# Performance work log

Measured on AMD Instinct MI355X. Metric: run time of the kernel, lower is better.

Reference implementation:

```python
import jax, jax.numpy as jnp
import numpy as np

ITER_ROUTING = 3
EPS = 1e-9


def squash(s):
    # s: [C, H]; standard capsule squash along last dim
    norm_sq = jnp.sum(s * s, axis=-1, keepdims=True)
    return s * (norm_sq / (1.0 + norm_sq)) / jnp.sqrt(norm_sq + EPS)


def setup_inputs() -> dict:
    key = jax.random.key(0)
    k1, k2 = jax.random.split(key)
    C, K, H = 512, 64, 1024
    encoder_output = jax.random.normal(k1, (C, K, H), dtype=jnp.float32)
    # nn.Linear(H, H, bias=False) weight, scaled like kaiming-uniform-ish init
    W = jax.random.normal(k2, (H, H), dtype=jnp.float32) * (1.0 / np.sqrt(H))
    return {"encoder_output": encoder_output, "W": W}


def reference(encoder_output, W):
    C, K, H = encoder_output.shape
    # Linear projection (loop-invariant: l_1 is fixed, so hoist out of routing loop)
    # torch Linear computes x @ W.T
    hat = jnp.einsum('ckh,oh->cko', encoder_output, W)  # [C, K, H]
    b = jnp.zeros((C, K), dtype=encoder_output.dtype)
    c = None
    for _ in range(ITER_ROUTING):
        d = jax.nn.softmax(b, axis=-1)                  # [C, K]
        c_hat = jnp.einsum('ckh,ck->ch', hat, d)        # [C, H] weighted sum
        c = squash(c_hat)                               # [C, H]
        b = b + jnp.einsum('ckh,ch->ck', hat, c)        # agreement update
    return c
```

## Files before the change

### kernel.cpp

```cpp
#include <hip/hip_runtime.h>
#include <hip/hip_bf16.h>
#include <cstdint>


#define C_DIM 512
#define KCAPS 64
#define H_DIM 1024
#define M_DIM (C_DIM * KCAPS)

typedef _Float16 h8 __attribute__((ext_vector_type(8)));
typedef _Float16 h4 __attribute__((ext_vector_type(4)));
typedef float f4 __attribute__((ext_vector_type(4)));

__global__ void cvt_f32_f16(const float* __restrict__ in, _Float16* __restrict__ out, int n4) {
    int i = blockIdx.x * blockDim.x + threadIdx.x;
    int stride = gridDim.x * blockDim.x;
    for (; i < n4; i += stride) {
        float4 v = ((const float4*)in)[i];
        h4 o;
        o[0] = (_Float16)v.x; o[1] = (_Float16)v.y;
        o[2] = (_Float16)v.z; o[3] = (_Float16)v.w;
        ((h4*)out)[i] = o;
    }
}

__device__ __forceinline__ void gload16(const _Float16* g, _Float16* l) {
    __builtin_amdgcn_global_load_lds(
        (const __attribute__((address_space(1))) void*)g,
        (__attribute__((address_space(3))) void*)l, 16, 0, 0);
}

__global__ __launch_bounds__(256) void gemm_f16_bt(const _Float16* __restrict__ A,
                                                   const _Float16* __restrict__ B,
                                                   _Float16* __restrict__ Cmat) {
    __shared__ _Float16 As[128 * 64] __attribute__((aligned(16)));
    __shared__ _Float16 Bs[128 * 64] __attribute__((aligned(16)));
    const int tid  = threadIdx.x;
    const int lane = tid & 63;
    const int wid  = tid >> 6;
    const int bid  = blockIdx.x;
    const int swz  = (bid & 7) * 256 + (bid >> 3);
    const int tm   = swz >> 3;
    const int tn   = swz & 7;
    const int wr   = wid >> 1, wc = wid & 1;

    f4 acc[4][4] = {};

    const int r8 = lane >> 3;
    const int c8 = (lane & 7) * 8;

    const _Float16* Abase = A + (size_t)(tm * 128) * H_DIM;
    const _Float16* Bbase = B + (size_t)(tn * 128) * H_DIM;

    for (int kt = 0; kt < H_DIM; kt += 64) {
        #pragma unroll
        for (int i = 0; i < 4; ++i) {
            const int chunk = wid * 4 + i;
            const int row   = chunk * 8 + r8;
            gload16(Abase + (size_t)row * H_DIM + kt + c8, &As[chunk * 512]);
            gload16(Bbase + (size_t)row * H_DIM + kt + c8, &Bs[chunk * 512]);
        }
        __syncthreads();

        #pragma unroll
        for (int kk = 0; kk < 64; kk += 32) {
            h8 af[4], bf[4];
            const int kidx = kk + ((lane >> 4) << 3);
            #pragma unroll
            for (int m = 0; m < 4; ++m)
                af[m] = *(const h8*)&As[(wr * 64 + m * 16 + (lane & 15)) * 64 + kidx];
            #pragma unroll
            for (int n = 0; n < 4; ++n)
                bf[n] = *(const h8*)&Bs[(wc * 64 + n * 16 + (lane & 15)) * 64 + kidx];
            #pragma unroll
            for (int m = 0; m < 4; ++m)
                #pragma unroll
                for (int n = 0; n < 4; ++n)
                    acc[m][n] = __builtin_amdgcn_mfma_f32_16x16x32_f16(af[m], bf[n], acc[m][n], 0, 0, 0);
        }
        __syncthreads();
    }

    const int crow0 = tm * 128 + wr * 64;
    const int ccol0 = tn * 128 + wc * 64;
    #pragma unroll
    for (int m = 0; m < 4; ++m) {
        #pragma unroll
        for (int n = 0; n < 4; ++n) {
            const int col = ccol0 + n * 16 + (lane & 15);
            #pragma unroll
            for (int q = 0; q < 4; ++q) {
                const int row = crow0 + m * 16 + (lane >> 4) * 4 + q;
                Cmat[(size_t)row * H_DIM + col] = (_Float16)acc[m][n][q];
            }
        }
    }
}

__device__ __forceinline__ float2 upk(unsigned int u) {
    unsigned short ul = (unsigned short)(u & 0xffffu);
    unsigned short uh = (unsigned short)(u >> 16);
    _Float16 lo, hi;
    __builtin_memcpy(&lo, &ul, 2);
    __builtin_memcpy(&hi, &uh, 2);
    return make_float2((float)lo, (float)hi);
}

__global__ __launch_bounds__(512) void routing2(const _Float16* __restrict__ hat,
                                                float* __restrict__ out) {
    __shared__ _Float16 hat_s[KCAPS * H_DIM] __attribute__((aligned(16)));
    __shared__ float b_lds[KCAPS];
    __shared__ float d_lds[KCAPS];
    __shared__ float c_lds[H_DIM];
    __shared__ float red[8];
    __shared__ float norm_sh;

    const int c    = blockIdx.x;
    const int t    = threadIdx.x;
    const int lane = t & 63;
    const int wid  = t >> 6;

    const _Float16* gbase = hat + (size_t)c * (KCAPS * H_DIM);
    #pragma unroll
    for (int i = 0; i < 16; ++i) {
        const int chunk = wid * 16 + i;
        gload16(gbase + chunk * 512 + lane * 8, &hat_s[chunk * 512]);
    }
    if (t < 64) b_lds[t] = 0.0f;
    __syncthreads();

    float cx = 0.0f, cy = 0.0f;

    for (int it = 0; it < 3; ++it) {
        if (wid == 0) {
            float bv = b_lds[lane];
            float mx = bv;
            #pragma unroll
            for (int s = 1; s < 64; s <<= 1) mx = fmaxf(mx, __shfl_xor(mx, s, 64));
            float e = __expf(bv - mx);
            float sum = e;
            #pragma unroll
            for (int s = 1; s < 64; s <<= 1) sum += __shfl_xor(sum, s, 64);
            d_lds[lane] = e / sum;
        }
        __syncthreads();

        float chx = 0.0f, chy = 0.0f;
        #pragma unroll
        for (int k = 0; k < 64; ++k) {
            unsigned int u = *(const unsigned int*)&hat_s[k * H_DIM + 2 * t];
            float2 f = upk(u);
            float dk = d_lds[k];
            chx = fmaf(f.x, dk, chx);
            chy = fmaf(f.y, dk, chy);
        }

        float nn = chx * chx + chy * chy;
        #pragma unroll
        for (int s = 1; s < 64; s <<= 1) nn += __shfl_xor(nn, s, 64);
        if (lane == 0) red[wid] = nn;
        __syncthreads();
        if (t == 0) {
            float tot = 0.0f;
            #pragma unroll
            for (int w = 0; w < 8; ++w) tot += red[w];
            norm_sh = tot;
        }
        __syncthreads();
        const float ns = norm_sh;
        const float scale = (ns / (1.0f + ns)) / sqrtf(ns + 1e-9f);
        cx = chx * scale;
        cy = chy * scale;

        if (it == 2) break;

        c_lds[2 * t]     = cx;
        c_lds[2 * t + 1] = cy;
        __syncthreads();

        float4 cc[4];
        #pragma unroll
        for (int q = 0; q < 4; ++q)
            cc[q] = *(const float4*)&c_lds[lane * 16 + q * 4];

        #pragma unroll
        for (int j = 0; j < 8; ++j) {
            const int k = wid * 8 + j;
            const h8* hp = (const h8*)&hat_s[k * H_DIM + lane * 16];
            float p = 0.0f;
            #pragma unroll
            for (int half = 0; half < 2; ++half) {
                h8 v = hp[half];
                const float* cf = (const float*)&cc[half * 2];
                #pragma unroll
                for (int e = 0; e < 8; ++e)
                    p = fmaf((float)v[e], cf[e], p);
            }
            #pragma unroll
            for (int s = 1; s < 64; s <<= 1) p += __shfl_xor(p, s, 64);
            if (lane == 0) b_lds[k] += p;
        }
        __syncthreads();
    }

    float2 o;
    o.x = cx; o.y = cy;
    *(float2*)&out[(size_t)c * H_DIM + 2 * t] = o;
}

extern "C" void kernel_launch(void* const* d_in, const int* in_sizes, int n_in,
                              void* d_out, int out_size, void* d_ws, size_t ws_size,
                              hipStream_t stream) {
    const float* enc = (const float*)d_in[0];
    const float* Wf  = (const float*)d_in[1];
    float* out = (float*)d_out;

    char* ws = (char*)d_ws;
    _Float16* enc16 = (_Float16*)ws;
    _Float16* W16   = (_Float16*)(ws + (size_t)67108864);
    _Float16* hat16 = (_Float16*)(ws + (size_t)67108864 + 2097152);

    const int n_enc = C_DIM * KCAPS * H_DIM;
    const int n_w   = H_DIM * H_DIM;

    cvt_f32_f16<<<2048, 256, 0, stream>>>(enc, enc16, n_enc / 4);
    cvt_f32_f16<<<512, 256, 0, stream>>>(Wf, W16, n_w / 4);

    gemm_f16_bt<<<(M_DIM / 128) * (H_DIM / 128), 256, 0, stream>>>(enc16, W16, hat16);

    routing2<<<C_DIM, 512, 0, stream>>>(hat16, out);
}
```

Baseline: 336.9 us.

## Fuse projection GEMM into routing kernel, computing hat per capsule in LDS

Drops the separate encoder fp32-to-fp16 conversion, the standalone GEMM and the global hat buffer. Each routing block now reads its capsule's fp32 encoder slice, converts it on the fly into LDS, and runs MFMA against fp16 W read directly from global memory, writing the 64x1024 hat tile straight into LDS. This removes the global write and re-read of the 64MB hat intermediate and two launches. In exchange, W is re-read from global/L2 by all 512 blocks with no LDS staging, there are only 512 blocks, and the large LDS footprint limits occupancy. The agreement dot-product loop is also re-indexed to read interleaved LDS addresses.

```diff
diff --git a/kernel.cpp b/kernel.cpp
--- a/kernel.cpp
+++ b/kernel.cpp
@@ -6,7 +6,6 @@
 #define C_DIM 512
 #define KCAPS 64
 #define H_DIM 1024
-#define M_DIM (C_DIM * KCAPS)
 
 typedef _Float16 h8 __attribute__((ext_vector_type(8)));
 typedef _Float16 h4 __attribute__((ext_vector_type(4)));
@@ -24,79 +23,6 @@
     }
 }
 
-__device__ __forceinline__ void gload16(const _Float16* g, _Float16* l) {
-    __builtin_amdgcn_global_load_lds(
-        (const __attribute__((address_space(1))) void*)g,
-        (__attribute__((address_space(3))) void*)l, 16, 0, 0);
-}
-
-__global__ __launch_bounds__(256) void gemm_f16_bt(const _Float16* __restrict__ A,
-                                                   const _Float16* __restrict__ B,
-                                                   _Float16* __restrict__ Cmat) {
-    __shared__ _Float16 As[128 * 64] __attribute__((aligned(16)));
-    __shared__ _Float16 Bs[128 * 64] __attribute__((aligned(16)));
-    const int tid  = threadIdx.x;
-    const int lane = tid & 63;
-    const int wid  = tid >> 6;
-    const int bid  = blockIdx.x;
-    const int swz  = (bid & 7) * 256 + (bid >> 3);
-    const int tm   = swz >> 3;
-    const int tn   = swz & 7;
-    const int wr   = wid >> 1, wc = wid & 1;
-
-    f4 acc[4][4] = {};
-
-    const int r8 = lane >> 3;
-    const int c8 = (lane & 7) * 8;
-
-    const _Float16* Abase = A + (size_t)(tm * 128) * H_DIM;
-    const _Float16* Bbase = B + (size_t)(tn * 128) * H_DIM;
-
-    for (int kt = 0; kt < H_DIM; kt += 64) {
-        #pragma unroll
-        for (int i = 0; i < 4; ++i) {
-            const int chunk = wid * 4 + i;
-            const int row   = chunk * 8 + r8;
-            gload16(Abase + (size_t)row * H_DIM + kt + c8, &As[chunk * 512]);
-            gload16(Bbase + (size_t)row * H_DIM + kt + c8, &Bs[chunk * 512]);
-        }
-        __syncthreads();
-
-        #pragma unroll
-        for (int kk = 0; kk < 64; kk += 32) {
-            h8 af[4], bf[4];
-            const int kidx = kk + ((lane >> 4) << 3);
-            #pragma unroll
-            for (int m = 0; m < 4; ++m)
-                af[m] = *(const h8*)&As[(wr * 64 + m * 16 + (lane & 15)) * 64 + kidx];
-            #pragma unroll
-            for (int n = 0; n < 4; ++n)
-                bf[n] = *(const h8*)&Bs[(wc * 64 + n * 16 + (lane & 15)) * 64 + kidx];
-            #pragma unroll
-            for (int m = 0; m < 4; ++m)
-                #pragma unroll
-                for (int n = 0; n < 4; ++n)
-                    acc[m][n] = __builtin_amdgcn_mfma_f32_16x16x32_f16(af[m], bf[n], acc[m][n], 0, 0, 0);
-        }
-        __syncthreads();
-    }
-
-    const int crow0 = tm * 128 + wr * 64;
-    const int ccol0 = tn * 128 + wc * 64;
-    #pragma unroll
-    for (int m = 0; m < 4; ++m) {
-        #pragma unroll
-        for (int n = 0; n < 4; ++n) {
-            const int col = ccol0 + n * 16 + (lane & 15);
-            #pragma unroll
-            for (int q = 0; q < 4; ++q) {
-                const int row = crow0 + m * 16 + (lane >> 4) * 4 + q;
-                Cmat[(size_t)row * H_DIM + col] = (_Float16)acc[m][n][q];
-            }
-        }
-    }
-}
-
 __device__ __forceinline__ float2 upk(unsigned int u) {
     unsigned short ul = (unsigned short)(u & 0xffffu);
     unsigned short uh = (unsigned short)(u >> 16);
@@ -106,12 +32,14 @@
     return make_float2((float)lo, (float)hi);
 }
 
-__global__ __launch_bounds__(512) void routing2(const _Float16* __restrict__ hat,
-                                                float* __restrict__ out) {
+__global__ __launch_bounds__(512, 2) void fused_caps(const float* __restrict__ enc,
+                                                     const _Float16* __restrict__ W16,
+                                                     float* __restrict__ out) {
     __shared__ _Float16 hat_s[KCAPS * H_DIM] __attribute__((aligned(16)));
+    __shared__ _Float16 As[8 * 64 * 8] __attribute__((aligned(16)));
+    __shared__ float c_lds[H_DIM];
     __shared__ float b_lds[KCAPS];
     __shared__ float d_lds[KCAPS];
-    __shared__ float c_lds[H_DIM];
     __shared__ float red[8];
     __shared__ float norm_sh;
 
@@ -120,13 +48,69 @@
     const int lane = t & 63;
     const int wid  = t >> 6;
 
-    const _Float16* gbase = hat + (size_t)c * (KCAPS * H_DIM);
+    const float*     Aenc = enc + (size_t)c * (KCAPS * H_DIM);
+    const _Float16*  Wb   = W16 + (size_t)(wid * 128) * H_DIM;
+
+    const int arow = t >> 3;
+    const int akgr = t & 7;
+    const float* aptr = Aenc + arow * H_DIM + akgr * 8;
+
+    if (t < KCAPS) b_lds[t] = 0.0f;
+
+    f4 acc[4][8] = {};
+
+    float4 pre0 = *(const float4*)(aptr);
+    float4 pre1 = *(const float4*)(aptr + 4);
+
+    for (int kt = 0; kt < H_DIM; kt += 64) {
+        __syncthreads();
+        {
+            h8 av;
+            av[0] = (_Float16)pre0.x; av[1] = (_Float16)pre0.y;
+            av[2] = (_Float16)pre0.z; av[3] = (_Float16)pre0.w;
+            av[4] = (_Float16)pre1.x; av[5] = (_Float16)pre1.y;
+            av[6] = (_Float16)pre1.z; av[7] = (_Float16)pre1.w;
+            *(h8*)&As[akgr * 512 + arow * 8] = av;
+        }
+        if (kt + 64 < H_DIM) {
+            pre0 = *(const float4*)(aptr + kt + 64);
+            pre1 = *(const float4*)(aptr + kt + 64 + 4);
+        }
+        __syncthreads();
+
+        #pragma unroll
+        for (int s = 0; s < 2; ++s) {
+            const int kq = (lane >> 4);
+            h8 bf[8];
+            #pragma unroll
+            for (int n = 0; n < 8; ++n)
+                bf[n] = *(const h8*)(Wb + (size_t)(n * 16 + (lane & 15)) * H_DIM
+                                     + kt + s * 32 + kq * 8);
+            h8 af[4];
+            #pragma unroll
+            for (int m = 0; m < 4; ++m)
+                af[m] = *(const h8*)&As[(s * 4 + kq) * 512 + (m * 16 + (lane & 15)) * 8];
+            #pragma unroll
+            for (int m = 0; m < 4; ++m)
+                #pragma unroll
+                for (int n = 0; n < 8; ++n)
+                    acc[m][n] = __builtin_amdgcn_mfma_f32_16x16x32_f16(af[m], bf[n], acc[m][n], 0, 0, 0);
+        }
+    }
+
+    __syncthreads();
     #pragma unroll
-    for (int i = 0; i < 16; ++i) {
-        const int chunk = wid * 16 + i;
-        gload16(gbase + chunk * 512 + lane * 8, &hat_s[chunk * 512]);
-    }
-    if (t < 64) b_lds[t] = 0.0f;
+    for (int m = 0; m < 4; ++m) {
+        #pragma unroll
+        for (int n = 0; n < 8; ++n) {
+            const int col = wid * 128 + n * 16 + (lane & 15);
+            #pragma unroll
+            for (int q = 0; q < 4; ++q) {
+                const int row = m * 16 + (lane >> 4) * 4 + q;
+                hat_s[row * H_DIM + col] = (_Float16)acc[m][n][q];
+            }
+        }
+    }
     __syncthreads();
 
     float cx = 0.0f, cy = 0.0f;
@@ -178,23 +162,18 @@
         c_lds[2 * t + 1] = cy;
         __syncthreads();
 
-        float4 cc[4];
-        #pragma unroll
-        for (int q = 0; q < 4; ++q)
-            cc[q] = *(const float4*)&c_lds[lane * 16 + q * 4];
-
         #pragma unroll
         for (int j = 0; j < 8; ++j) {
             const int k = wid * 8 + j;
-            const h8* hp = (const h8*)&hat_s[k * H_DIM + lane * 16];
             float p = 0.0f;
             #pragma unroll
-            for (int half = 0; half < 2; ++half) {
-                h8 v = hp[half];
-                const float* cf = (const float*)&cc[half * 2];
-                #pragma unroll
-                for (int e = 0; e < 8; ++e)
-                    p = fmaf((float)v[e], cf[e], p);
+            for (int i = 0; i < 8; ++i) {
+                const int hp = lane + 64 * i;
+                unsigned int u = *(const unsigned int*)&hat_s[k * H_DIM + 2 * hp];
+                float2 f = upk(u);
+                float2 cc = *(const float2*)&c_lds[2 * hp];
+                p = fmaf(f.x, cc.x, p);
+                p = fmaf(f.y, cc.y, p);
             }
             #pragma unroll
             for (int s = 1; s < 64; s <<= 1) p += __shfl_xor(p, s, 64);
@@ -215,18 +194,10 @@
     const float* Wf  = (const float*)d_in[1];
     float* out = (float*)d_out;
 
-    char* ws = (char*)d_ws;
-    _Float16* enc16 = (_Float16*)ws;
-    _Float16* W16   = (_Float16*)(ws + (size_t)67108864);
-    _Float16* hat16 = (_Float16*)(ws + (size_t)67108864 + 2097152);
-
-    const int n_enc = C_DIM * KCAPS * H_DIM;
-    const int n_w   = H_DIM * H_DIM;
-
-    cvt_f32_f16<<<2048, 256, 0, stream>>>(enc, enc16, n_enc / 4);
+    _Float16* W16 = (_Float16*)d_ws;
+
+    const int n_w = H_DIM * H_DIM;
+
     cvt_f32_f16<<<512, 256, 0, stream>>>(Wf, W16, n_w / 4);
-
-    gemm_f16_bt<<<(M_DIM / 128) * (H_DIM / 128), 256, 0, stream>>>(enc16, W16, hat16);
-
-    routing2<<<C_DIM, 512, 0, stream>>>(hat16, out);
-}
+    fused_caps<<<C_DIM, 512, 0, stream>>>(enc, W16, out);
+}
```

After: 331.1 us. About the same (-1.7%).
